# Optimization experiments

Measured on AMD Instinct MI355X. Metric: run time of the kernel, lower is better.

The kernel has to match this reference:

```python
import jax, jax.numpy as jnp
import numpy as np

NQ = 20
P_MAX = 480 * 640 - 1  # hardcoded clamp in original module


def make_quantizer_params(nq=NQ, mn=0.0, mx=1.0):
    # Replicates APLoss.__init__ conv1d weight/bias initialization.
    a = (nq - 1) / (mx - mn)
    w = np.concatenate([-a * np.ones(nq), a * np.ones(nq)]).astype(np.float32)
    b = np.concatenate([a * mn + np.arange(nq, 0, -1),
                        np.arange(2 - nq, 2, 1) - a * mn]).astype(np.float32)
    w[0] = w[-1] = 0.0
    b[0] = b[-1] = 1.0
    return jnp.asarray(w), jnp.asarray(b)


def setup_inputs() -> dict:
    key = jax.random.key(0)
    k1, k2, k3, k4, k5 = jax.random.split(key, 5)
    P, D, N, NEG = 307200, 64, 20000, 80
    qw, qb = make_quantizer_params()
    return {
        "descriptors1": jax.random.normal(k1, (1, P, D), dtype=jnp.float32),
        "descriptors2": jax.random.normal(k2, (1, P, D), dtype=jnp.float32),
        "qw": qw,
        "qb": qb,
        "matches_1": jax.random.randint(k3, (N,), 0, P),
        "matches_2": jax.random.randint(k4, (N,), 0, P),
        "offsets": jax.random.randint(k5, (NEG,), 0, 640),
    }


def reference(descriptors1, descriptors2, qw, qb, matches_1, matches_2, offsets):
    nq = qw.shape[0] // 2
    d1 = descriptors1[0]  # (P, D)
    d2 = descriptors2[0]  # (P, D)

    # negative indices: offset positive matches, clamp to valid pixel range
    non_m2 = jnp.clip(matches_2[:, None] + offsets[None, :], 0, P_MAX)  # (N, NEG)

    a1 = d1[matches_1]                                  # (N, D)
    pos = jnp.sum(a1 * d2[matches_2], axis=-1)          # (N,)
    neg = jnp.einsum('nd,nmd->nm', a1, d2[non_m2])      # (N, NEG)

    scores = jnp.concatenate([pos[:, None], neg], axis=1)   # (N, M), M = 1+NEG
    label = jnp.zeros_like(scores).at[:, 0].set(1.0)         # (N, M)

    # soft quantizer: 1x1 conv == per-bin affine; min of two halves, relu
    x = scores[:, None, :]                                   # (N, 1, M)
    q = jnp.minimum(qw[:nq, None] * x + qb[:nq, None],
                    qw[nq:, None] * x + qb[nq:, None])
    q = jnp.maximum(q, 0.0)                                  # (N, nq, M)

    nbs = q.sum(axis=-1)                                     # (N, nq)
    rec = (q * label[:, None, :]).sum(axis=-1)               # (N, nq)
    prec = jnp.cumsum(rec, axis=-1) / (1e-16 + jnp.cumsum(nbs, axis=-1))
    rec = rec / rec.sum(axis=-1, keepdims=True)
    ap = (prec * rec).sum(axis=-1)                           # (N,)
    return (1.0 - ap).mean()
```

## Files before the change

kernel.cpp:

```cpp
#include <hip/hip_runtime.h>

#define DIM 64
#define MAXBUCK 2560
#define SORT_T 1024

__global__ __launch_bounds__(1024) void k_sort(const int* __restrict__ m2,
                                               int* __restrict__ perm, int N, int nbuck)
{
    __shared__ int cnt[MAXBUCK];
    __shared__ int s[SORT_T];
    const int tid = threadIdx.x;

    for (int i = tid; i < nbuck; i += SORT_T) cnt[i] = 0;
    __syncthreads();
    for (int i = tid; i < N; i += SORT_T) atomicAdd(&cnt[m2[i] >> 7], 1);
    __syncthreads();

    const int base = tid * 3;
    int loc[3];
    int sum = 0;
    #pragma unroll
    for (int u = 0; u < 3; ++u) {
        const int idx = base + u;
        const int v = (idx < nbuck) ? cnt[idx] : 0;
        loc[u] = sum;
        sum += v;
    }
    s[tid] = sum;
    __syncthreads();
    for (int off = 1; off < SORT_T; off <<= 1) {
        const int v = (tid >= off) ? s[tid - off] : 0;
        __syncthreads();
        s[tid] += v;
        __syncthreads();
    }
    const int excl = (tid > 0) ? s[tid - 1] : 0;
    #pragma unroll
    for (int u = 0; u < 3; ++u) {
        const int idx = base + u;
        if (idx < nbuck) cnt[idx] = excl + loc[u];
    }
    __syncthreads();
    for (int i = tid; i < N; i += SORT_T) {
        const int pos = atomicAdd(&cnt[m2[i] >> 7], 1);
        perm[pos] = i;
    }
}

__global__ __launch_bounds__(256) void pixel_ap_main(
    const float* __restrict__ d1, const float* __restrict__ d2,
    const float* __restrict__ qw, const float* __restrict__ qb,
    const int* __restrict__ m1, const int* __restrict__ m2,
    const int* __restrict__ offs, const int* __restrict__ perm,
    float* __restrict__ partial, int P, int NEG, int NQ2, int N)
{
    const int tid  = threadIdx.x;
    const int wave = tid >> 6;
    const int lane = tid & 63;
    const int nq   = NQ2 >> 1;
    const int M    = NEG + 1;

    __shared__ int   s_off[128];
    __shared__ float s_scores[4][96];

    if (tid < NEG) s_off[tid] = offs[tid];
    __syncthreads();

    const int b    = blockIdx.x;
    const int per  = (gridDim.x + 7) >> 3;
    const int pos  = (b & 7) * per + (b >> 3);
    const int sid0 = pos * 4 + wave;
    const int sid  = min(sid0, N - 1);

    const int n  = perm[sid];
    const int i1 = m1[n];
    const int i2 = m2[n];

    const int g = lane >> 4;
    const int l = lane & 15;
    const float4 a4 = ((const float4*)(d1 + (size_t)i1 * DIM))[l];

    for (int c = 0; c < 3; ++c) {
        float4 bv[7];
        #pragma unroll
        for (int u = 0; u < 7; ++u) {
            const int j = g + 4 * (7 * c + u);
            if (j < M) {
                const int row = (j == 0) ? i2 : min(i2 + s_off[j - 1], P - 1);
                bv[u] = ((const float4*)(d2 + (size_t)row * DIM))[l];
            }
        }
        #pragma unroll
        for (int u = 0; u < 7; ++u) {
            const int j = g + 4 * (7 * c + u);
            if (j < M) {
                float sd = bv[u].x * a4.x + bv[u].y * a4.y + bv[u].z * a4.z + bv[u].w * a4.w;
                sd += __shfl_xor(sd, 1);
                sd += __shfl_xor(sd, 2);
                sd += __shfl_xor(sd, 4);
                sd += __shfl_xor(sd, 8);
                if (l == 0) s_scores[wave][j] = sd;
            }
        }
    }
    __syncthreads();

    const float a_scale = qw[nq];
    const float amn     = qb[nq - 1] - 1.0f;
    const float ulim    = (float)(nq - 1);

    const float xp = s_scores[wave][0];
    const float up = fminf(fmaxf(a_scale * xp - amn, 0.0f), ulim);
    const float ip = floorf(up);
    const float fp = up - ip;

    float n1 = 0.0f, n2 = 0.0f;
    if (lane < M) {
        const float x  = s_scores[wave][lane];
        const float u  = fminf(fmaxf(a_scale * x - amn, 0.0f), ulim);
        const float fi = floorf(u);
        const float f  = u - fi;
        n2 += (fi >= ip)        ? 1.0f : ((fi == ip - 1.0f) ? f : 0.0f);
        n1 += (fi >= ip + 1.0f) ? 1.0f : ((fi == ip)        ? f : 0.0f);
    }
    const int j2 = lane + 64;
    if (j2 < M) {
        const float x  = s_scores[wave][j2];
        const float u  = fminf(fmaxf(a_scale * x - amn, 0.0f), ulim);
        const float fi = floorf(u);
        const float f  = u - fi;
        n2 += (fi >= ip)        ? 1.0f : ((fi == ip - 1.0f) ? f : 0.0f);
        n1 += (fi >= ip + 1.0f) ? 1.0f : ((fi == ip)        ? f : 0.0f);
    }
    #pragma unroll
    for (int off = 32; off >= 1; off >>= 1) {
        n1 += __shfl_xor(n1, off);
        n2 += __shfl_xor(n2, off);
    }
    if (lane == 0 && sid0 < N) {
        const float ap = fp * fp / (1e-16f + n1) + (1.0f - fp) / (1e-16f + n2);
        partial[n] = 1.0f - ap;
    }
}

__global__ __launch_bounds__(1024) void k_reduce(const float* __restrict__ partial,
                                                 float* __restrict__ out, int N)
{
    float s = 0.0f;
    for (int i = threadIdx.x; i < N; i += 1024) s += partial[i];
    #pragma unroll
    for (int off = 32; off >= 1; off >>= 1) s += __shfl_xor(s, off);
    __shared__ float sw[16];
    if ((threadIdx.x & 63) == 0) sw[threadIdx.x >> 6] = s;
    __syncthreads();
    if (threadIdx.x == 0) {
        float t = 0.0f;
        #pragma unroll
        for (int w = 0; w < 16; ++w) t += sw[w];
        out[0] = t / (float)N;
    }
}

extern "C" void kernel_launch(void* const* d_in, const int* in_sizes, int n_in,
                              void* d_out, int out_size, void* d_ws, size_t ws_size,
                              hipStream_t stream) {
    const float* d1   = (const float*)d_in[0];
    const float* d2   = (const float*)d_in[1];
    const float* qw   = (const float*)d_in[2];
    const float* qb   = (const float*)d_in[3];
    const int*   m1   = (const int*)d_in[4];
    const int*   m2   = (const int*)d_in[5];
    const int*   offs = (const int*)d_in[6];

    const int N     = in_sizes[4];
    const int P     = in_sizes[0] / DIM;
    const int NEG   = in_sizes[6];
    const int NQ2   = in_sizes[2];
    const int nbuck = (P + 127) >> 7;

    int*   perm    = (int*)d_ws;
    float* partial = (float*)(perm + N);

    k_sort<<<1, SORT_T, 0, stream>>>(m2, perm, N, nbuck);

    const int nb = (N + 3) / 4;
    pixel_ap_main<<<nb, 256, 0, stream>>>(d1, d2, qw, qb, m1, m2, offs, perm,
                                          partial, P, NEG, NQ2, N);

    k_reduce<<<1, 1024, 0, stream>>>(partial, (float*)d_out, N);
}
```

Measured before the change: 222.2 us.

## Assign one match per 256-thread block with 8-lane dot-product groups

```diff
diff --git a/kernel.cpp b/kernel.cpp
--- a/kernel.cpp
+++ b/kernel.cpp
@@ -54,53 +54,61 @@
     const int* __restrict__ offs, const int* __restrict__ perm,
     float* __restrict__ partial, int P, int NEG, int NQ2, int N)
 {
-    const int tid  = threadIdx.x;
-    const int wave = tid >> 6;
-    const int lane = tid & 63;
-    const int nq   = NQ2 >> 1;
-    const int M    = NEG + 1;
+    const int tid = threadIdx.x;
+    const int nq  = NQ2 >> 1;
+    const int M   = NEG + 1;
 
-    __shared__ int   s_off[128];
-    __shared__ float s_scores[4][96];
+    __shared__ int   s_row[96];
+    __shared__ float s_scores[96];
+    __shared__ float s_red[8];
 
-    if (tid < NEG) s_off[tid] = offs[tid];
-    __syncthreads();
+    const int b   = blockIdx.x;
+    const int per = (gridDim.x + 7) >> 3;
+    int pos = (b & 7) * per + (b >> 3);
+    if (pos >= N) pos = N - 1;
 
-    const int b    = blockIdx.x;
-    const int per  = (gridDim.x + 7) >> 3;
-    const int pos  = (b & 7) * per + (b >> 3);
-    const int sid0 = pos * 4 + wave;
-    const int sid  = min(sid0, N - 1);
-
-    const int n  = perm[sid];
+    const int n  = perm[pos];
     const int i1 = m1[n];
     const int i2 = m2[n];
 
-    const int g = lane >> 4;
-    const int l = lane & 15;
-    const float4 a4 = ((const float4*)(d1 + (size_t)i1 * DIM))[l];
+    if (tid < M) {
+        s_row[tid] = (tid == 0) ? i2 : min(i2 + offs[tid - 1], P - 1);
+    }
+    __syncthreads();
 
-    for (int c = 0; c < 3; ++c) {
-        float4 bv[7];
-        #pragma unroll
-        for (int u = 0; u < 7; ++u) {
-            const int j = g + 4 * (7 * c + u);
-            if (j < M) {
-                const int row = (j == 0) ? i2 : min(i2 + s_off[j - 1], P - 1);
-                bv[u] = ((const float4*)(d2 + (size_t)row * DIM))[l];
-            }
+    const int g  = tid >> 3;
+    const int sl = tid & 7;
+
+    const float* a_ptr = d1 + (size_t)i1 * DIM + 8 * sl;
+    const float4 a0 = ((const float4*)a_ptr)[0];
+    const float4 a1 = ((const float4*)a_ptr)[1];
+
+    int rows[3];
+    #pragma unroll
+    for (int t = 0; t < 3; ++t) {
+        const int j = g + 32 * t;
+        rows[t] = s_row[(j < M) ? j : 0];
+    }
+    float4 b0[3], b1[3];
+    #pragma unroll
+    for (int t = 0; t < 3; ++t) {
+        const int j = g + 32 * t;
+        if (j < M) {
+            const float* p = d2 + (size_t)rows[t] * DIM + 8 * sl;
+            b0[t] = ((const float4*)p)[0];
+            b1[t] = ((const float4*)p)[1];
         }
-        #pragma unroll
-        for (int u = 0; u < 7; ++u) {
-            const int j = g + 4 * (7 * c + u);
-            if (j < M) {
-                float sd = bv[u].x * a4.x + bv[u].y * a4.y + bv[u].z * a4.z + bv[u].w * a4.w;
-                sd += __shfl_xor(sd, 1);
-                sd += __shfl_xor(sd, 2);
-                sd += __shfl_xor(sd, 4);
-                sd += __shfl_xor(sd, 8);
-                if (l == 0) s_scores[wave][j] = sd;
-            }
+    }
+    #pragma unroll
+    for (int t = 0; t < 3; ++t) {
+        const int j = g + 32 * t;
+        if (j < M) {
+            float s = b0[t].x * a0.x + b0[t].y * a0.y + b0[t].z * a0.z + b0[t].w * a0.w
+                    + b1[t].x * a1.x + b1[t].y * a1.y + b1[t].z * a1.z + b1[t].w * a1.w;
+            s += __shfl_xor(s, 1);
+            s += __shfl_xor(s, 2);
+            s += __shfl_xor(s, 4);
+            if (sl == 0) s_scores[j] = s;
         }
     }
     __syncthreads();
@@ -109,36 +117,32 @@
     const float amn     = qb[nq - 1] - 1.0f;
     const float ulim    = (float)(nq - 1);
 
-    const float xp = s_scores[wave][0];
+    const float xp = s_scores[0];
     const float up = fminf(fmaxf(a_scale * xp - amn, 0.0f), ulim);
     const float ip = floorf(up);
     const float fp = up - ip;
 
     float n1 = 0.0f, n2 = 0.0f;
-    if (lane < M) {
-        const float x  = s_scores[wave][lane];
+    if (tid < M) {
+        const float x  = s_scores[tid];
         const float u  = fminf(fmaxf(a_scale * x - amn, 0.0f), ulim);
         const float fi = floorf(u);
         const float f  = u - fi;
-        n2 += (fi >= ip)        ? 1.0f : ((fi == ip - 1.0f) ? f : 0.0f);
-        n1 += (fi >= ip + 1.0f) ? 1.0f : ((fi == ip)        ? f : 0.0f);
-    }
-    const int j2 = lane + 64;
-    if (j2 < M) {
-        const float x  = s_scores[wave][j2];
-        const float u  = fminf(fmaxf(a_scale * x - amn, 0.0f), ulim);
-        const float fi = floorf(u);
-        const float f  = u - fi;
-        n2 += (fi >= ip)        ? 1.0f : ((fi == ip - 1.0f) ? f : 0.0f);
-        n1 += (fi >= ip + 1.0f) ? 1.0f : ((fi == ip)        ? f : 0.0f);
+        n2 = (fi >= ip)        ? 1.0f : ((fi == ip - 1.0f) ? f : 0.0f);
+        n1 = (fi >= ip + 1.0f) ? 1.0f : ((fi == ip)        ? f : 0.0f);
     }
     #pragma unroll
     for (int off = 32; off >= 1; off >>= 1) {
         n1 += __shfl_xor(n1, off);
         n2 += __shfl_xor(n2, off);
     }
-    if (lane == 0 && sid0 < N) {
-        const float ap = fp * fp / (1e-16f + n1) + (1.0f - fp) / (1e-16f + n2);
+    const int wid = tid >> 6;
+    if ((tid & 63) == 0) { s_red[wid] = n1; s_red[4 + wid] = n2; }
+    __syncthreads();
+    if (tid == 0) {
+        const float N1 = s_red[0] + s_red[1] + s_red[2] + s_red[3];
+        const float N2 = s_red[4] + s_red[5] + s_red[6] + s_red[7];
+        const float ap = fp * fp / (1e-16f + N1) + (1.0f - fp) / (1e-16f + N2);
         partial[n] = 1.0f - ap;
     }
 }
@@ -183,9 +187,8 @@
 
     k_sort<<<1, SORT_T, 0, stream>>>(m2, perm, N, nbuck);
 
-    const int nb = (N + 3) / 4;
-    pixel_ap_main<<<nb, 256, 0, stream>>>(d1, d2, qw, qb, m1, m2, offs, perm,
-                                          partial, P, NEG, NQ2, N);
+    pixel_ap_main<<<N, 256, 0, stream>>>(d1, d2, qw, qb, m1, m2, offs, perm,
+                                         partial, P, NEG, NQ2, N);
 
     k_reduce<<<1, 1024, 0, stream>>>(partial, (float*)d_out, N);
 }
```

Measured after the change: 210.2 us. 5.4% less time.
